# Optimization experiments

Hardware: AMD Instinct MI355X
Metric: run time of the kernel (lower is better)

Reference implementation:

```python
import jax, jax.numpy as jnp
import numpy as np

N_NODES = 100_000
N_EDGES = 1_600_000
IN_CH = 128
HIDDEN = 48
OUT_CH = 16
NEG_SLOPE = 0.2  # PyG GATConv default LeakyReLU slope


def setup_inputs() -> dict:
    key = jax.random.key(0)
    ks = jax.random.split(key, 8)
    x = jax.random.normal(ks[0], (N_NODES, IN_CH), dtype=jnp.float32)
    edge_index = jax.random.randint(ks[1], (2, N_EDGES), 0, N_NODES, dtype=jnp.int64)
    W = jax.random.normal(ks[2], (IN_CH, HIDDEN), dtype=jnp.float32) / np.sqrt(IN_CH)
    att_src = jax.random.normal(ks[3], (HIDDEN,), dtype=jnp.float32) / np.sqrt(HIDDEN)
    att_dst = jax.random.normal(ks[4], (HIDDEN,), dtype=jnp.float32) / np.sqrt(HIDDEN)
    gat_bias = jax.random.normal(ks[5], (HIDDEN,), dtype=jnp.float32) * 0.01
    lin_W = jax.random.normal(ks[6], (HIDDEN, OUT_CH), dtype=jnp.float32) / np.sqrt(HIDDEN)
    lin_b = jax.random.normal(ks[7], (OUT_CH,), dtype=jnp.float32) * 0.01
    return {"x": x, "edge_index": edge_index, "W": W, "att_src": att_src,
            "att_dst": att_dst, "gat_bias": gat_bias, "lin_W": lin_W, "lin_b": lin_b}


def reference(x, edge_index, W, att_src, att_dst, gat_bias, lin_W, lin_b):
    n = x.shape[0]
    # PyG GATConv adds self loops by default
    loops = jnp.arange(n, dtype=edge_index.dtype)
    src = jnp.concatenate([edge_index[0], loops])  # [E+N] message sources j
    dst = jnp.concatenate([edge_index[1], loops])  # [E+N] message targets i

    h = x @ W                      # [N, H] transformed node features
    a_src = h @ att_src            # [N] per-node source attention term
    a_dst = h @ att_dst            # [N] per-node destination attention term

    logits = jax.nn.leaky_relu(a_src[src] + a_dst[dst], NEG_SLOPE)  # [E+N]
    # segment softmax over incoming edges of each destination node
    m = jax.ops.segment_max(logits, dst, num_segments=n)            # [N]
    e = jnp.exp(logits - m[dst])
    denom = jax.ops.segment_sum(e, dst, num_segments=n)             # [N] (>0: self loop)
    alpha = e / denom[dst]                                          # [E+N]

    agg = jax.ops.segment_sum(h[src] * alpha[:, None], dst, num_segments=n)
    out = jax.nn.elu(agg + gat_bias)          # [N, H]
    # dropout is identity in eval mode
    z = out @ lin_W + lin_b                   # [N, OUT]
    return jax.nn.log_softmax(z, axis=-1)
```

## Files before the change

kernel.cpp:

```cpp
#include <hip/hip_runtime.h>
#include <hip/hip_fp16.h>

#define IN_CH 128
#define HID 48
#define OUT_CH 16
#define NEG_SLOPE 0.2f
#define SCAN_ELEMS 2048
#define ROWB 128
#define WLP 20

__device__ __forceinline__ float leaky(float x) { return x >= 0.f ? x : NEG_SLOPE * x; }
__device__ __forceinline__ float elu(float x) { return x > 0.f ? x : __expf(x) - 1.f; }

__device__ __forceinline__ void load_edge(const void* ei, int E, int is64, int e,
                                          int& s, int& d) {
    if (is64) {
        const long long* p = (const long long*)ei;
        s = (int)p[e];
        d = (int)p[(size_t)E + e];
    } else {
        const int* p = (const int*)ei;
        s = p[e];
        d = p[(size_t)E + e];
    }
}

#define BLK_NODES 256
__global__ __launch_bounds__(256, 2) void k_xw(const float* __restrict__ x,
                                               const float* __restrict__ W,
                                               const float* __restrict__ att_src,
                                               const float* __restrict__ att_dst,
                                               const unsigned* __restrict__ ei,
                                               __half* __restrict__ h2,
                                               float* __restrict__ a_src,
                                               float* __restrict__ a_dst,
                                               int* __restrict__ deg,
                                               int* __restrict__ flag, int N) {
    __shared__ float Wl[IN_CH * HID];
    __shared__ float xl[BLK_NODES * 33];
    const int t = threadIdx.x;
    if (blockIdx.x == 0 && t == 0) {
        unsigned sdet = 0;
        for (int i = 1; i < 128; i += 2) sdet |= ei[i];
        *flag = (sdet == 0) ? 1 : 0;
    }
    for (int i = t; i < IN_CH * HID / 4; i += 256)
        ((float4*)Wl)[i] = ((const float4*)W)[i];
    const int n0 = blockIdx.x * BLK_NODES;
    const int kq = t & 3;
    const int ng = t >> 2;
    const int k0 = kq * 12;

    float acc[4][12];
#pragma unroll
    for (int i = 0; i < 4; ++i)
#pragma unroll
        for (int j = 0; j < 12; ++j) acc[i][j] = 0.f;

    for (int c0 = 0; c0 < IN_CH; c0 += 32) {
        __syncthreads();
#pragma unroll
        for (int p = 0; p < 8; ++p) {
            int id = t + p * 256;
            int row = id >> 3;
            int seg = id & 7;
            int n = n0 + row;
            float4 v = make_float4(0.f, 0.f, 0.f, 0.f);
            if (n < N) v = ((const float4*)(x + (size_t)n * IN_CH + c0))[seg];
            float* dst = &xl[row * 33 + seg * 4];
            dst[0] = v.x; dst[1] = v.y; dst[2] = v.z; dst[3] = v.w;
        }
        __syncthreads();
#pragma unroll 8
        for (int cc = 0; cc < 32; ++cc) {
            int c = c0 + cc;
            float xv[4];
#pragma unroll
            for (int i = 0; i < 4; ++i) xv[i] = xl[(ng * 4 + i) * 33 + cc];
            const float* wr = &Wl[c * HID + k0];
#pragma unroll
            for (int j = 0; j < 12; ++j) {
                float wv = wr[j];
#pragma unroll
                for (int i = 0; i < 4; ++i) acc[i][j] += xv[i] * wv;
            }
        }
    }
#pragma unroll
    for (int i = 0; i < 4; ++i) {
        int n = n0 + ng * 4 + i;
        if (n < N) {
            uint* dst = (uint*)((char*)h2 + (size_t)n * ROWB) + k0 / 2;
#pragma unroll
            for (int j = 0; j < 6; ++j) {
                __half2 hv = __floats2half2_rn(acc[i][2 * j], acc[i][2 * j + 1]);
                dst[j] = *(const uint*)&hv;
            }
        }
    }
#pragma unroll
    for (int p = 0; p < 8; ++p) {
        int id = t + p * 256;
        int row = id >> 3;
        int seg = id & 7;
        int n = n0 + row;
        if (n < N) ((uint*)((char*)h2 + (size_t)n * ROWB))[24 + seg] = 0u;
    }
    float as_[4], ad_[4];
#pragma unroll
    for (int i = 0; i < 4; ++i) {
        float s1 = 0.f, s2 = 0.f;
#pragma unroll
        for (int j = 0; j < 12; ++j) {
            float a = acc[i][j];
            s1 += a * att_src[k0 + j];
            s2 += a * att_dst[k0 + j];
        }
        s1 += __shfl_xor(s1, 1); s1 += __shfl_xor(s1, 2);
        s2 += __shfl_xor(s2, 1); s2 += __shfl_xor(s2, 2);
        as_[i] = s1; ad_[i] = s2;
    }
    if (kq == 0) {
#pragma unroll
        for (int i = 0; i < 4; ++i) {
            int n = n0 + ng * 4 + i;
            if (n < N) { a_src[n] = as_[i]; a_dst[n] = ad_[i]; }
        }
    }
    {
        int n = n0 + t;
        if (n < N) deg[n] = 0;
    }
}

__global__ __launch_bounds__(256) void k_count(const void* __restrict__ ei,
                                               const int* __restrict__ flag,
                                               int* __restrict__ deg,
                                               unsigned short* __restrict__ rank, int E) {
    int e = blockIdx.x * blockDim.x + threadIdx.x;
    if (e >= E) return;
    int d = (*flag) ? (int)((const long long*)ei)[(size_t)E + e]
                    : ((const int*)ei)[(size_t)E + e];
    rank[e] = (unsigned short)atomicAdd(&deg[d], 1);
}

__global__ __launch_bounds__(256) void k_scan_block(const int* __restrict__ deg,
                                                    int* __restrict__ rowptr,
                                                    int* __restrict__ bsum, int N) {
    __shared__ int sm[256];
    const int t = threadIdx.x;
    const int base = blockIdx.x * SCAN_ELEMS + t * 8;
    int v[8];
    int s = 0;
#pragma unroll
    for (int i = 0; i < 8; ++i) {
        v[i] = (base + i < N) ? deg[base + i] : 0;
        s += v[i];
    }
    sm[t] = s;
    __syncthreads();
    for (int off = 1; off < 256; off <<= 1) {
        int y = (t >= off) ? sm[t - off] : 0;
        __syncthreads();
        sm[t] += y;
        __syncthreads();
    }
    int run = sm[t] - s;
#pragma unroll
    for (int i = 0; i < 8; ++i) {
        if (base + i < N) rowptr[base + i] = run;
        run += v[i];
    }
    if (t == 255) bsum[blockIdx.x] = sm[255];
}

__global__ __launch_bounds__(256) void k_scan_add(int* __restrict__ rowptr,
                                                  const int* __restrict__ bsum, int N, int E) {
    __shared__ int soff;
    const int chunk = (int)(((long long)blockIdx.x * 256) / SCAN_ELEMS);
    if (threadIdx.x == 0) {
        int run = 0;
        for (int b = 0; b < chunk; ++b) run += bsum[b];
        soff = run;
    }
    __syncthreads();
    int i = blockIdx.x * 256 + threadIdx.x;
    if (i == 0) rowptr[N] = E;
    if (i >= N) return;
    rowptr[i] += soff;
}

__global__ __launch_bounds__(256) void k_scatter(const void* __restrict__ ei,
                                                 const int* __restrict__ flag,
                                                 const int* __restrict__ rowptr,
                                                 const unsigned short* __restrict__ rank,
                                                 unsigned* __restrict__ srcs, int E) {
    int e = blockIdx.x * blockDim.x + threadIdx.x;
    if (e >= E) return;
    int is64 = *flag;
    int s, d;
    load_edge(ei, E, is64, e, s, d);
    int pos = rowptr[d] + (int)rank[e];
    srcs[pos] = (unsigned)s;
}

__global__ __launch_bounds__(256) void k_gat_node(const int* __restrict__ rowptr,
                                                  const unsigned* __restrict__ srcs,
                                                  const float* __restrict__ a_src,
                                                  const float* __restrict__ a_dst,
                                                  const __half* __restrict__ h2,
                                                  const float* __restrict__ gat_bias,
                                                  const float* __restrict__ lin_W,
                                                  const float* __restrict__ lin_b,
                                                  float* __restrict__ out, int N) {
    __shared__ float Wl[HID * WLP];
    __shared__ float lb[OUT_CH];
    __shared__ float gb[HID];
    __shared__ float o_sm[4][HID];
    __shared__ unsigned long long evb[4][64];
    const int t = threadIdx.x;
    for (int i = t; i < HID * OUT_CH; i += 256) Wl[(i >> 4) * WLP + (i & 15)] = lin_W[i];
    if (t < OUT_CH) lb[t] = lin_b[t];
    if (t >= 64 && t < 64 + HID) gb[t - 64] = gat_bias[t - 64];
    __syncthreads();

    const int wv = t >> 6;
    const int lane = t & 63;
    const int slot = lane >> 4;
    const int c = lane & 15;
    const int n = blockIdx.x * 4 + wv;
    const bool active = n < N;

    if (active) {
        const int base = rowptr[n];
        const int deg = rowptr[n + 1] - base;
        const float adn = a_dst[n];
        const float ev_self = __expf(fminf(leaky(a_src[n] + adn), 50.f));
        const char* hb = (const char*)h2;

        float a0 = 0.f, a1 = 0.f, a2 = 0.f, a3 = 0.f;
        float evsum = (lane == 0) ? ev_self : 0.f;
        if (slot == 0) {
            uint2 hv = *(const uint2*)(hb + (size_t)n * ROWB + 8 * c);
            __half2 h01 = *(const __half2*)&hv.x;
            __half2 h23 = *(const __half2*)&hv.y;
            a0 = ev_self * __low2float(h01);
            a1 = ev_self * __high2float(h01);
            a2 = ev_self * __low2float(h23);
            a3 = ev_self * __high2float(h23);
        }
        for (int c0 = 0; c0 < deg; c0 += 64) {
            int j = c0 + lane;
            unsigned s = 0;
            float ev = 0.f;
            if (j < deg) {
                s = srcs[base + j];
                ev = __expf(fminf(leaky(a_src[s] + adn), 50.f));
            }
            evsum += ev;
            evb[wv][lane] = ((unsigned long long)__float_as_uint(ev) << 32) | s;
            const int cnt = (deg - c0 < 64) ? (deg - c0) : 64;
            int jj = slot;
            unsigned long long prA = 0;
            uint2 hvA = make_uint2(0u, 0u);
            if (jj < cnt) {
                prA = evb[wv][jj];
                hvA = *(const uint2*)(hb + (size_t)(unsigned)prA * ROWB + 8 * c);
            }
#pragma unroll 2
            for (; jj + 4 < cnt; jj += 4) {
                unsigned long long prB = evb[wv][jj + 4];
                uint2 hvB = *(const uint2*)(hb + (size_t)(unsigned)prB * ROWB + 8 * c);
                float evj = __uint_as_float((unsigned)(prA >> 32));
                __half2 h01 = *(const __half2*)&hvA.x;
                __half2 h23 = *(const __half2*)&hvA.y;
                a0 += evj * __low2float(h01);
                a1 += evj * __high2float(h01);
                a2 += evj * __low2float(h23);
                a3 += evj * __high2float(h23);
                prA = prB; hvA = hvB;
            }
            if (jj < cnt) {
                float evj = __uint_as_float((unsigned)(prA >> 32));
                __half2 h01 = *(const __half2*)&hvA.x;
                __half2 h23 = *(const __half2*)&hvA.y;
                a0 += evj * __low2float(h01);
                a1 += evj * __high2float(h01);
                a2 += evj * __low2float(h23);
                a3 += evj * __high2float(h23);
            }
        }
#pragma unroll
        for (int off = 1; off < 64; off <<= 1) evsum += __shfl_xor(evsum, off);
        a0 += __shfl_xor(a0, 16); a0 += __shfl_xor(a0, 32);
        a1 += __shfl_xor(a1, 16); a1 += __shfl_xor(a1, 32);
        a2 += __shfl_xor(a2, 16); a2 += __shfl_xor(a2, 32);
        a3 += __shfl_xor(a3, 16); a3 += __shfl_xor(a3, 32);
        const float inv = 1.f / evsum;
        if (slot == 0 && c < 12) {
            float4 v = make_float4(elu(a0 * inv + gb[4 * c + 0]),
                                   elu(a1 * inv + gb[4 * c + 1]),
                                   elu(a2 * inv + gb[4 * c + 2]),
                                   elu(a3 * inv + gb[4 * c + 3]));
            *(float4*)&o_sm[wv][4 * c] = v;
        }
    }
    __syncthreads();

    if (active) {
        const float* o = o_sm[wv];
        float z = 0.f;
#pragma unroll
        for (int i = 0; i < 12; ++i) {
            int k = 12 * slot + i;
            z += o[k] * Wl[k * WLP + c];
        }
        z += __shfl_xor(z, 16); z += __shfl_xor(z, 32);
        z += lb[c];
        float mx = z;
#pragma unroll
        for (int off = 8; off; off >>= 1) mx = fmaxf(mx, __shfl_xor(mx, off, 16));
        float ev = __expf(z - mx);
#pragma unroll
        for (int off = 8; off; off >>= 1) ev += __shfl_xor(ev, off, 16);
        float lse = mx + __logf(ev);
        if (slot == 0) out[(size_t)n * OUT_CH + c] = z - lse;
    }
}

extern "C" void kernel_launch(void* const* d_in, const int* in_sizes, int n_in,
                              void* d_out, int out_size, void* d_ws, size_t ws_size,
                              hipStream_t stream) {
    const float* x = (const float*)d_in[0];
    const void* edge_index = d_in[1];
    const float* W = (const float*)d_in[2];
    const float* att_src = (const float*)d_in[3];
    const float* att_dst = (const float*)d_in[4];
    const float* gat_bias = (const float*)d_in[5];
    const float* lin_W = (const float*)d_in[6];
    const float* lin_b = (const float*)d_in[7];
    float* out = (float*)d_out;

    const int N = in_sizes[0] / IN_CH;
    const int E = in_sizes[1] / 2;

    __half* h2 = (__half*)d_ws;
    float* a_src = (float*)((char*)d_ws + (size_t)N * ROWB);
    float* a_dst = a_src + N;
    int* rowptr = (int*)(a_dst + N);
    int* degbuf = rowptr + N + 1;
    int* bsum = degbuf + N;
    int* flag = bsum + 64;
    unsigned short* rank = (unsigned short*)(flag + 1);
    unsigned* srcs =
        (unsigned*)(((uintptr_t)(rank + E) + 3) & ~(uintptr_t)3);

    const int nodeBlocks = (N + 255) / 256;
    const int edgeBlocks = (E + 255) / 256;
    const int scanBlocks = (N + SCAN_ELEMS - 1) / SCAN_ELEMS;

    k_xw<<<(N + BLK_NODES - 1) / BLK_NODES, 256, 0, stream>>>(
        x, W, att_src, att_dst, (const unsigned*)edge_index,
        h2, a_src, a_dst, degbuf, flag, N);
    k_count<<<edgeBlocks, 256, 0, stream>>>(edge_index, flag, degbuf, rank, E);
    k_scan_block<<<scanBlocks, 256, 0, stream>>>(degbuf, rowptr, bsum, N);
    k_scan_add<<<nodeBlocks, 256, 0, stream>>>(rowptr, bsum, N, E);
    k_scatter<<<edgeBlocks, 256, 0, stream>>>(edge_index, flag, rowptr, rank, srcs, E);
    k_gat_node<<<(N + 3) / 4, 256, 0, stream>>>(rowptr, srcs, a_src, a_dst,
                                                h2, gat_bias, lin_W, lin_b, out, N);
}
```

Before: 208.2 us.

## Restructure x@W tile per wave, vectorize edge count and scatter kernels

The x@W kernel now assigns each wave one 12-column slice of W, which is read as wave-uniform scalar loads instead of staged through shared memory. x is stored transposed in shared memory so each lane reads four nodes with one float4. The attention dot products are reduced through shared memory rather than lane shuffles, and occupancy is raised to 3 blocks per CU. The count and scatter kernels each handle four edges per thread using vector loads of the edge indices and ranks, cutting thread count and load instructions at the cost of less parallelism for the atomics and writes.

```diff
diff --git a/kernel.cpp b/kernel.cpp
--- a/kernel.cpp
+++ b/kernel.cpp
@@ -8,6 +8,7 @@
 #define SCAN_ELEMS 2048
 #define ROWB 128
 #define WLP 20
+#define XLS 260
 
 __device__ __forceinline__ float leaky(float x) { return x >= 0.f ? x : NEG_SLOPE * x; }
 __device__ __forceinline__ float elu(float x) { return x > 0.f ? x : __expf(x) - 1.f; }
@@ -26,7 +27,7 @@
 }
 
 #define BLK_NODES 256
-__global__ __launch_bounds__(256, 2) void k_xw(const float* __restrict__ x,
+__global__ __launch_bounds__(256, 3) void k_xw(const float* __restrict__ x,
                                                const float* __restrict__ W,
                                                const float* __restrict__ att_src,
                                                const float* __restrict__ att_dst,
@@ -36,20 +37,18 @@
                                                float* __restrict__ a_dst,
                                                int* __restrict__ deg,
                                                int* __restrict__ flag, int N) {
-    __shared__ float Wl[IN_CH * HID];
-    __shared__ float xl[BLK_NODES * 33];
+    __shared__ float xl[32 * XLS];
+    __shared__ float asl[2][4][BLK_NODES];
     const int t = threadIdx.x;
     if (blockIdx.x == 0 && t == 0) {
         unsigned sdet = 0;
         for (int i = 1; i < 128; i += 2) sdet |= ei[i];
         *flag = (sdet == 0) ? 1 : 0;
     }
-    for (int i = t; i < IN_CH * HID / 4; i += 256)
-        ((float4*)Wl)[i] = ((const float4*)W)[i];
     const int n0 = blockIdx.x * BLK_NODES;
-    const int kq = t & 3;
-    const int ng = t >> 2;
-    const int k0 = kq * 12;
+    const int wv = t >> 6;
+    const int lane = t & 63;
+    const int k0u = __builtin_amdgcn_readfirstlane(wv * 12);
 
     float acc[4][12];
 #pragma unroll
@@ -67,30 +66,33 @@
             int n = n0 + row;
             float4 v = make_float4(0.f, 0.f, 0.f, 0.f);
             if (n < N) v = ((const float4*)(x + (size_t)n * IN_CH + c0))[seg];
-            float* dst = &xl[row * 33 + seg * 4];
-            dst[0] = v.x; dst[1] = v.y; dst[2] = v.z; dst[3] = v.w;
+            float* dst = &xl[(seg * 4) * XLS + row];
+            dst[0 * XLS] = v.x; dst[1 * XLS] = v.y;
+            dst[2 * XLS] = v.z; dst[3 * XLS] = v.w;
         }
         __syncthreads();
-#pragma unroll 8
+#pragma unroll 4
         for (int cc = 0; cc < 32; ++cc) {
-            int c = c0 + cc;
-            float xv[4];
-#pragma unroll
-            for (int i = 0; i < 4; ++i) xv[i] = xl[(ng * 4 + i) * 33 + cc];
-            const float* wr = &Wl[c * HID + k0];
+            const float* wr = &W[(size_t)(c0 + cc) * HID + k0u];
+            float wv12[12];
+#pragma unroll
+            for (int j = 0; j < 12; ++j) wv12[j] = wr[j];
+            float4 xv = *(const float4*)&xl[cc * XLS + 4 * lane];
 #pragma unroll
             for (int j = 0; j < 12; ++j) {
-                float wv = wr[j];
-#pragma unroll
-                for (int i = 0; i < 4; ++i) acc[i][j] += xv[i] * wv;
+                float wvj = wv12[j];
+                acc[0][j] += xv.x * wvj;
+                acc[1][j] += xv.y * wvj;
+                acc[2][j] += xv.z * wvj;
+                acc[3][j] += xv.w * wvj;
             }
         }
     }
 #pragma unroll
     for (int i = 0; i < 4; ++i) {
-        int n = n0 + ng * 4 + i;
+        int n = n0 + lane * 4 + i;
         if (n < N) {
-            uint* dst = (uint*)((char*)h2 + (size_t)n * ROWB) + k0 / 2;
+            uint* dst = (uint*)((char*)h2 + (size_t)n * ROWB) + k0u / 2;
 #pragma unroll
             for (int j = 0; j < 6; ++j) {
                 __half2 hv = __floats2half2_rn(acc[i][2 * j], acc[i][2 * j + 1]);
@@ -106,30 +108,35 @@
         int n = n0 + row;
         if (n < N) ((uint*)((char*)h2 + (size_t)n * ROWB))[24 + seg] = 0u;
     }
-    float as_[4], ad_[4];
-#pragma unroll
-    for (int i = 0; i < 4; ++i) {
-        float s1 = 0.f, s2 = 0.f;
-#pragma unroll
-        for (int j = 0; j < 12; ++j) {
-            float a = acc[i][j];
-            s1 += a * att_src[k0 + j];
-            s2 += a * att_dst[k0 + j];
-        }
-        s1 += __shfl_xor(s1, 1); s1 += __shfl_xor(s1, 2);
-        s2 += __shfl_xor(s2, 1); s2 += __shfl_xor(s2, 2);
-        as_[i] = s1; ad_[i] = s2;
-    }
-    if (kq == 0) {
+    {
+        float s1[4], s2[4];
+        float as12[12], ad12[12];
+#pragma unroll
+        for (int j = 0; j < 12; ++j) { as12[j] = att_src[k0u + j]; ad12[j] = att_dst[k0u + j]; }
 #pragma unroll
         for (int i = 0; i < 4; ++i) {
-            int n = n0 + ng * 4 + i;
-            if (n < N) { a_src[n] = as_[i]; a_dst[n] = ad_[i]; }
-        }
-    }
+            float u = 0.f, v = 0.f;
+#pragma unroll
+            for (int j = 0; j < 12; ++j) {
+                u += acc[i][j] * as12[j];
+                v += acc[i][j] * ad12[j];
+            }
+            s1[i] = u; s2[i] = v;
+        }
+#pragma unroll
+        for (int i = 0; i < 4; ++i) {
+            asl[0][wv][lane * 4 + i] = s1[i];
+            asl[1][wv][lane * 4 + i] = s2[i];
+        }
+    }
+    __syncthreads();
     {
         int n = n0 + t;
-        if (n < N) deg[n] = 0;
+        if (n < N) {
+            a_src[n] = asl[0][0][t] + asl[0][1][t] + asl[0][2][t] + asl[0][3][t];
+            a_dst[n] = asl[1][0][t] + asl[1][1][t] + asl[1][2][t] + asl[1][3][t];
+            deg[n] = 0;
+        }
     }
 }
 
@@ -137,11 +144,33 @@
                                                const int* __restrict__ flag,
                                                int* __restrict__ deg,
                                                unsigned short* __restrict__ rank, int E) {
-    int e = blockIdx.x * blockDim.x + threadIdx.x;
-    if (e >= E) return;
-    int d = (*flag) ? (int)((const long long*)ei)[(size_t)E + e]
-                    : ((const int*)ei)[(size_t)E + e];
-    rank[e] = (unsigned short)atomicAdd(&deg[d], 1);
+    int e0 = 4 * (blockIdx.x * blockDim.x + threadIdx.x);
+    if (e0 >= E) return;
+    int is64 = *flag;
+    if (e0 + 3 < E) {
+        int d[4];
+        if (is64) {
+            const long long* p = (const long long*)ei;
+            longlong4 v = *(const longlong4*)&p[(size_t)E + e0];
+            d[0] = (int)v.x; d[1] = (int)v.y; d[2] = (int)v.z; d[3] = (int)v.w;
+        } else {
+            const int* p = (const int*)ei;
+            int4 v = *(const int4*)&p[(size_t)E + e0];
+            d[0] = v.x; d[1] = v.y; d[2] = v.z; d[3] = v.w;
+        }
+        ushort4 r;
+        r.x = (unsigned short)atomicAdd(&deg[d[0]], 1);
+        r.y = (unsigned short)atomicAdd(&deg[d[1]], 1);
+        r.z = (unsigned short)atomicAdd(&deg[d[2]], 1);
+        r.w = (unsigned short)atomicAdd(&deg[d[3]], 1);
+        *(ushort4*)&rank[e0] = r;
+    } else {
+        for (int e = e0; e < E; ++e) {
+            int d = is64 ? (int)((const long long*)ei)[(size_t)E + e]
+                         : ((const int*)ei)[(size_t)E + e];
+            rank[e] = (unsigned short)atomicAdd(&deg[d], 1);
+        }
+    }
 }
 
 __global__ __launch_bounds__(256) void k_scan_block(const int* __restrict__ deg,
@@ -195,13 +224,36 @@
                                                  const int* __restrict__ rowptr,
                                                  const unsigned short* __restrict__ rank,
                                                  unsigned* __restrict__ srcs, int E) {
-    int e = blockIdx.x * blockDim.x + threadIdx.x;
-    if (e >= E) return;
+    int e0 = 4 * (blockIdx.x * blockDim.x + threadIdx.x);
+    if (e0 >= E) return;
     int is64 = *flag;
-    int s, d;
-    load_edge(ei, E, is64, e, s, d);
-    int pos = rowptr[d] + (int)rank[e];
-    srcs[pos] = (unsigned)s;
+    if (e0 + 3 < E) {
+        int s[4], d[4];
+        if (is64) {
+            const long long* p = (const long long*)ei;
+            longlong4 vs = *(const longlong4*)&p[e0];
+            longlong4 vd = *(const longlong4*)&p[(size_t)E + e0];
+            s[0] = (int)vs.x; s[1] = (int)vs.y; s[2] = (int)vs.z; s[3] = (int)vs.w;
+            d[0] = (int)vd.x; d[1] = (int)vd.y; d[2] = (int)vd.z; d[3] = (int)vd.w;
+        } else {
+            const int* p = (const int*)ei;
+            int4 vs = *(const int4*)&p[e0];
+            int4 vd = *(const int4*)&p[(size_t)E + e0];
+            s[0] = vs.x; s[1] = vs.y; s[2] = vs.z; s[3] = vs.w;
+            d[0] = vd.x; d[1] = vd.y; d[2] = vd.z; d[3] = vd.w;
+        }
+        ushort4 r = *(const ushort4*)&rank[e0];
+        srcs[rowptr[d[0]] + (int)r.x] = (unsigned)s[0];
+        srcs[rowptr[d[1]] + (int)r.y] = (unsigned)s[1];
+        srcs[rowptr[d[2]] + (int)r.z] = (unsigned)s[2];
+        srcs[rowptr[d[3]] + (int)r.w] = (unsigned)s[3];
+    } else {
+        for (int e = e0; e < E; ++e) {
+            int s, d;
+            load_edge(ei, E, is64, e, s, d);
+            srcs[rowptr[d] + (int)rank[e]] = (unsigned)s;
+        }
+    }
 }
 
 __global__ __launch_bounds__(256) void k_gat_node(const int* __restrict__ rowptr,
@@ -356,16 +408,16 @@
         (unsigned*)(((uintptr_t)(rank + E) + 3) & ~(uintptr_t)3);
 
     const int nodeBlocks = (N + 255) / 256;
-    const int edgeBlocks = (E + 255) / 256;
+    const int edge4Blocks = ((E + 3) / 4 + 255) / 256;
     const int scanBlocks = (N + SCAN_ELEMS - 1) / SCAN_ELEMS;
 
     k_xw<<<(N + BLK_NODES - 1) / BLK_NODES, 256, 0, stream>>>(
         x, W, att_src, att_dst, (const unsigned*)edge_index,
         h2, a_src, a_dst, degbuf, flag, N);
-    k_count<<<edgeBlocks, 256, 0, stream>>>(edge_index, flag, degbuf, rank, E);
+    k_count<<<edge4Blocks, 256, 0, stream>>>(edge_index, flag, degbuf, rank, E);
     k_scan_block<<<scanBlocks, 256, 0, stream>>>(degbuf, rowptr, bsum, N);
     k_scan_add<<<nodeBlocks, 256, 0, stream>>>(rowptr, bsum, N, E);
-    k_scatter<<<edgeBlocks, 256, 0, stream>>>(edge_index, flag, rowptr, rank, srcs, E);
+    k_scatter<<<edge4Blocks, 256, 0, stream>>>(edge_index, flag, rowptr, rank, srcs, E);
     k_gat_node<<<(N + 3) / 4, 256, 0, stream>>>(rowptr, srcs, a_src, a_dst,
                                                 h2, gat_bias, lin_W, lin_b, out, N);
 }
```

After: 219.9 us. +5.6%, slower.
